# Kernel tuning notes

Measured on AMD Instinct MI355X. Metric: run time of the kernel, lower is better.

## Reference

```python
import jax, jax.numpy as jnp
import numpy as np

N = 40000      # nodes (adj.size(0))
ISIZE = 64     # feature dim
K = 24         # kept kNN neighbors per node after d_cut mask
E = N * K      # learner candidate edges
E_ADJ = N * K  # GCN adjacency edges
OMEGA = 0.9
GAMMA = 2.0
D_CUT = 1.5


def setup_inputs() -> dict:
    key = jax.random.key(0)
    k = jax.random.split(key, 8)
    features = jax.random.normal(k[0], (N, ISIZE), jnp.float32)
    sc = 1.0 / np.sqrt(ISIZE)
    W1 = jax.random.normal(k[1], (ISIZE, ISIZE), jnp.float32) * sc
    b1 = jnp.zeros((ISIZE,), jnp.float32)
    W2 = jax.random.normal(k[2], (ISIZE, ISIZE), jnp.float32) * sc
    b2 = jnp.zeros((ISIZE,), jnp.float32)
    adj_row = jax.random.randint(k[3], (E_ADJ,), 0, N, dtype=jnp.int32)
    adj_col = jax.random.randint(k[4], (E_ADJ,), 0, N, dtype=jnp.int32)
    # kNN-style candidate edges: K neighbors per node, no self loops
    i_idx = jnp.repeat(jnp.arange(N, dtype=jnp.int32), K)
    j_idx = (i_idx + jax.random.randint(k[5], (E,), 1, N, dtype=jnp.int32)) % N
    # precomputed distance prior: s_d = 1/exp(gamma*(d/d_cut)^2)
    dist = jax.random.uniform(k[6], (E,), jnp.float32, 0.1, 2.0)
    s_d = jnp.exp(-GAMMA * (dist / D_CUT) ** 2)
    return {"features": features, "W1": W1, "b1": b1, "W2": W2, "b2": b2,
            "s_d": s_d, "adj_row": adj_row, "adj_col": adj_col,
            "i_idx": i_idx, "j_idx": j_idx}


def _gcn(x, W, b, row, col):
    """PyG GCNConv: symmetric norm with self loops, aggregate src=row into dst=col."""
    xw = x @ W
    deg = 1.0 + jax.ops.segment_sum(jnp.ones((row.shape[0],), jnp.float32), col,
                                    num_segments=N)
    dinv = jax.lax.rsqrt(deg)
    msg = (dinv[row] * dinv[col])[:, None] * xw[row]            # [E_ADJ, ISIZE]
    out = jax.ops.segment_sum(msg, col, num_segments=N)
    return out + (dinv * dinv)[:, None] * xw + b                # self-loop + bias


def reference(features, W1, b1, W2, b2, s_d, adj_row, adj_col, i_idx, j_idx):
    # GCN stack (nlayers=2), ReLU between layers
    h = jax.nn.relu(_gcn(features, W1, b1, adj_row, adj_col))
    h = _gcn(h, W2, b2, adj_row, adj_col)
    # F.normalize(h, p=2, dim=-1)
    h = h / jnp.maximum(jnp.linalg.norm(h, axis=-1, keepdims=True), 1e-12)
    # per-edge cosine scores, clamped at 0, blended with distance prior
    s_val = jnp.sum(h[i_idx] * h[j_idx], axis=-1)               # [E]
    s_val = jax.nn.relu(s_val)
    s_val = OMEGA * s_val + (1.0 - OMEGA) * s_d
    # SparseTensor.to_symmetric(reduce='mean'): average with reverse edge if present
    keys = i_idx * N + j_idx                                    # fits int32 (N=4e4)
    rkeys = j_idx * N + i_idx
    order = jnp.argsort(keys)
    sk = keys[order]
    pos = jnp.clip(jnp.searchsorted(sk, rkeys), 0, E - 1)
    found = sk[pos] == rkeys
    rev = order[pos]
    v_sym = jnp.where(found, 0.5 * (s_val + s_val[rev]), s_val)
    # symmetric COO: original edges + reverse copies (zeroed where reverse existed)
    rows_s = jnp.concatenate([i_idx, j_idx])                    # [2E]
    cols_s = jnp.concatenate([j_idx, i_idx])
    vals_s = jnp.concatenate([v_sym, jnp.where(found, 0.0, v_sym)])
    # normalize_adj_symm: D^{-1/2} S D^{-1/2}
    deg = jax.ops.segment_sum(vals_s, rows_s, num_segments=N)
    dinv = jnp.where(deg > 0, jax.lax.rsqrt(jnp.maximum(deg, 1e-12)), 0.0)
    vals_norm = dinv[rows_s] * vals_s * dinv[cols_s]
    return vals_norm, vals_s
```

## Files before the change

kernel.cpp:

```cpp
#include <hip/hip_runtime.h>

#define N_NODES 40000
#define ISIZE   64
#define KNN     24
#define NE      (N_NODES * KNN)
#define OMEGA   0.9f
#define CAP     64
#define NBUCK   80
#define BCAP    16384
#define JBCAP   16384
#define EPT     8

__device__ __forceinline__ float bf2f(unsigned short s) {
    return __uint_as_float(((unsigned)s) << 16);
}
__device__ __forceinline__ unsigned short f2bf(float f) {
    unsigned u = __float_as_uint(f);
    u += 0x7fffu + ((u >> 16) & 1u);
    return (unsigned short)(u >> 16);
}
__device__ __forceinline__ float bflo(unsigned u) { return __uint_as_float(u << 16); }
__device__ __forceinline__ float bfhi(unsigned u) { return __uint_as_float(u & 0xffff0000u); }
__device__ __forceinline__ unsigned pack2(float lo, float hi) {
    return (unsigned)f2bf(lo) | ((unsigned)f2bf(hi) << 16);
}

__global__ void k_mega1(const float* __restrict__ X, const float* __restrict__ W,
                        unsigned short* __restrict__ Y0, unsigned short* __restrict__ Y1,
                        const int* __restrict__ row, const int* __restrict__ col,
                        const int* __restrict__ j_idx,
                        int* __restrict__ bcnt, unsigned* __restrict__ bbuf,
                        unsigned* __restrict__ ovf2, int* __restrict__ ovf2_cnt,
                        int* __restrict__ jbcnt, unsigned* __restrict__ jbbuf,
                        unsigned* __restrict__ jovf, int* __restrict__ jovf_cnt,
                        unsigned char* __restrict__ revb) {
    __shared__ float sW[64 * 64];
    __shared__ float sX[32 * 64];
    const int GB  = N_NODES / 32;
    const int NBA = (NE + 256 * EPT - 1) / (256 * EPT);
    int bx = blockIdx.x;
    int tid = threadIdx.x;
    if (bx < GB) {
        int row0 = bx * 32;
        for (int t = tid; t < 1024; t += 256)
            ((float4*)sW)[t] = ((const float4*)W)[t];
        for (int t = tid; t < 512; t += 256)
            ((float4*)sX)[t] = ((const float4*)(X + row0 * 64))[t];
        __syncthreads();
        int cc = tid & 63;
        int rl = tid >> 6;
        for (int r = rl; r < 32; r += 4) {
            float acc = 0.0f;
#pragma unroll
            for (int kk = 0; kk < 64; kk++) acc += sX[r * 64 + kk] * sW[kk * 64 + cc];
            if (cc < 32) Y0[(row0 + r) * 32 + cc]      = f2bf(acc);
            else         Y1[(row0 + r) * 32 + cc - 32] = f2bf(acc);
        }
    } else if (bx < GB + 2 * NBA) {
        int* lcnt  = (int*)sW;
        int* lbase = lcnt + NBUCK;
        int blk = bx - GB;
        bool adj = blk < NBA;
        if (!adj) blk -= NBA;
        for (int b = tid; b < NBUCK; b += 256) lcnt[b] = 0;
        __syncthreads();
        int e0 = blk * (256 * EPT);
        int myslot[EPT]; int myb[EPT]; unsigned myp[EPT];
        for (int k = 0; k < EPT; k++) {
            int e = e0 + k * 256 + tid;
            if (e < NE) {
                int b; unsigned p;
                if (adj) { int r = row[e], c = col[e]; b = c >> 9; p = ((unsigned)r << 16) | (unsigned)c; }
                else     { int j = j_idx[e];           b = j >> 9; p = ((unsigned)(j & 511) << 20) | (unsigned)e; }
                myb[k] = b; myp[k] = p;
                myslot[k] = atomicAdd(&lcnt[b], 1);
            } else myb[k] = -1;
        }
        __syncthreads();
        int* gcnt = adj ? bcnt : jbcnt;
        for (int b = tid; b < NBUCK; b += 256)
            lbase[b] = (lcnt[b] > 0) ? atomicAdd(&gcnt[b], lcnt[b]) : 0;
        __syncthreads();
        unsigned* gbuf = adj ? bbuf : jbbuf;
        unsigned* govf = adj ? ovf2 : jovf;
        int* gocnt = adj ? ovf2_cnt : jovf_cnt;
        for (int k = 0; k < EPT; k++) {
            if (myb[k] < 0) continue;
            int pos = lbase[myb[k]] + myslot[k];
            if (pos < BCAP) gbuf[myb[k] * BCAP + pos] = myp[k];
            else { int p = atomicAdd(gocnt, 1); govf[p] = myp[k]; }
        }
    } else {
        int e = (bx - GB - 2 * NBA) * 256 + tid;
        int i = e / KNN;
        int j = j_idx[e];
        const uint4* jj4 = (const uint4*)(j_idx + j * KNN);
        int rt = 255;
#pragma unroll
        for (int k = 5; k >= 0; k--) {
            uint4 u = jj4[k];
            if ((int)u.w == i) rt = 4 * k + 3;
            if ((int)u.z == i) rt = 4 * k + 2;
            if ((int)u.y == i) rt = 4 * k + 1;
            if ((int)u.x == i) rt = 4 * k + 0;
        }
        revb[e] = (unsigned char)rt;
    }
}

__global__ void k_scatter3(const unsigned* __restrict__ bbuf, const int* __restrict__ bcnt,
                           int* __restrict__ cnt, unsigned short* __restrict__ ebuf,
                           unsigned* __restrict__ ovf, int* __restrict__ ovf_cnt,
                           const unsigned* __restrict__ ovf2, const int* __restrict__ ovf2_cnt) {
    __shared__ int lcnt2[512];
    int b = blockIdx.x;
    int tid = threadIdx.x;
    if (tid < 512) lcnt2[tid] = 0;
    __syncthreads();
    int n = min(bcnt[b], BCAP);
    for (int idx = tid; idx < n; idx += 1024) {
        unsigned p = bbuf[b * BCAP + idx];
        int c = (int)(p & 0xffffu), r = (int)(p >> 16);
        int slot = atomicAdd(&lcnt2[c & 511], 1);
        if (slot < CAP) ebuf[c * CAP + slot] = (unsigned short)r;
        else { int q = atomicAdd(ovf_cnt, 1); ovf[q] = p; }
    }
    int m = ovf2_cnt[0];
    for (int idx = tid; idx < m; idx += 1024) {
        unsigned p = ovf2[idx];
        int c = (int)(p & 0xffffu), r = (int)(p >> 16);
        if ((c >> 9) != b) continue;
        int slot = atomicAdd(&lcnt2[c & 511], 1);
        if (slot < CAP) ebuf[c * CAP + slot] = (unsigned short)r;
        else { int q = atomicAdd(ovf_cnt, 1); ovf[q] = p; }
    }
    __syncthreads();
    if (tid < 512) {
        int node = b * 512 + tid;
        if (node < N_NODES) cnt[node] = lcnt2[tid];
    }
}

__global__ void __launch_bounds__(1024, 1)
k_aggemm1(const uint4* __restrict__ X0q, const uint4* __restrict__ X1q,
          const float* __restrict__ W2,
          unsigned short* __restrict__ C0, unsigned short* __restrict__ C1,
          const int* __restrict__ cnt,
          const unsigned short* __restrict__ ebuf, const float* __restrict__ bias,
          const unsigned* __restrict__ ovf, const int* __restrict__ ovf_cnt) {
    __shared__ float sW[64 * 64];
    __shared__ float sB[32 * 64];
    int tid  = threadIdx.x;
    int lane = tid & 63;
    int half = lane >> 5, sl = lane & 31;
    int nl = (tid >> 6) * 2 + half;
    int n  = blockIdx.x * 32 + nl;

    ((float4*)sW)[tid] = ((const float4*)W2)[tid];

    int deg = cnt[n];
    int bucketed = min(deg, CAP);
    int nb0 = min(bucketed, 32);
    int nb1 = bucketed - nb0;

    int   r0v = 0, r1v = 0;
    float d0v = 0.0f, d1v = 0.0f;
    if (sl < nb0) { r0v = (int)ebuf[n * CAP + sl];      d0v = rsqrtf(1.0f + (float)cnt[r0v]); }
    if (sl < nb1) { r1v = (int)ebuf[n * CAP + 32 + sl]; d1v = rsqrtf(1.0f + (float)cnt[r1v]); }

    int g = sl >> 2;
    int f = sl & 3;

    float a[16];
#pragma unroll
    for (int k = 0; k < 16; k++) a[k] = 0.f;
    int np0 = (nb0 + 7) >> 3;
    int np1 = (nb1 + 7) >> 3;

#pragma unroll 4
    for (int d = 0; d < np0; d++) {
        int   q = 8 * d + g;
        int   r = __shfl(r0v, q, 32);
        float c = __shfl(d0v, q, 32);
        uint4 u0 = X0q[r * 4 + f];
        uint4 u1 = X1q[r * 4 + f];
        a[0]  += c * bflo(u0.x); a[1]  += c * bfhi(u0.x);
        a[2]  += c * bflo(u0.y); a[3]  += c * bfhi(u0.y);
        a[4]  += c * bflo(u0.z); a[5]  += c * bfhi(u0.z);
        a[6]  += c * bflo(u0.w); a[7]  += c * bfhi(u0.w);
        a[8]  += c * bflo(u1.x); a[9]  += c * bfhi(u1.x);
        a[10] += c * bflo(u1.y); a[11] += c * bfhi(u1.y);
        a[12] += c * bflo(u1.z); a[13] += c * bfhi(u1.z);
        a[14] += c * bflo(u1.w); a[15] += c * bfhi(u1.w);
    }
#pragma unroll 4
    for (int d = 0; d < np1; d++) {
        int   q = 8 * d + g;
        int   r = __shfl(r1v, q, 32);
        float c = __shfl(d1v, q, 32);
        uint4 u0 = X0q[r * 4 + f];
        uint4 u1 = X1q[r * 4 + f];
        a[0]  += c * bflo(u0.x); a[1]  += c * bfhi(u0.x);
        a[2]  += c * bflo(u0.y); a[3]  += c * bfhi(u0.y);
        a[4]  += c * bflo(u0.z); a[5]  += c * bfhi(u0.z);
        a[6]  += c * bflo(u0.w); a[7]  += c * bfhi(u0.w);
        a[8]  += c * bflo(u1.x); a[9]  += c * bfhi(u1.x);
        a[10] += c * bflo(u1.y); a[11] += c * bfhi(u1.y);
        a[12] += c * bflo(u1.z); a[13] += c * bfhi(u1.z);
        a[14] += c * bflo(u1.w); a[15] += c * bfhi(u1.w);
    }
    if (deg > CAP) {
        int m = ovf_cnt[0];
        for (int k2 = 0; k2 < m; k2++) {
            unsigned p = ovf[k2];
            if ((int)(p & 0xffffu) == n && g == 0) {
                int r = (int)(p >> 16);
                float c = rsqrtf(1.0f + (float)cnt[r]);
                uint4 u0 = X0q[r * 4 + f], u1 = X1q[r * 4 + f];
                a[0]  += c * bflo(u0.x); a[1]  += c * bfhi(u0.x);
                a[2]  += c * bflo(u0.y); a[3]  += c * bfhi(u0.y);
                a[4]  += c * bflo(u0.z); a[5]  += c * bfhi(u0.z);
                a[6]  += c * bflo(u0.w); a[7]  += c * bfhi(u0.w);
                a[8]  += c * bflo(u1.x); a[9]  += c * bfhi(u1.x);
                a[10] += c * bflo(u1.y); a[11] += c * bfhi(u1.y);
                a[12] += c * bflo(u1.z); a[13] += c * bfhi(u1.z);
                a[14] += c * bflo(u1.w); a[15] += c * bfhi(u1.w);
            }
        }
    }
#pragma unroll
    for (int k = 0; k < 16; k++) {
        a[k] += __shfl_xor(a[k], 4, 32);
        a[k] += __shfl_xor(a[k], 8, 32);
        a[k] += __shfl_xor(a[k], 16, 32);
    }

    float di = rsqrtf(1.0f + (float)deg);
    float dd = di * di;
    uint4 s0 = X0q[n * 4 + f], s1 = X1q[n * 4 + f];
    float4 bA0 = ((const float4*)bias)[2 * f];
    float4 bA1 = ((const float4*)bias)[2 * f + 1];
    float4 bB0 = ((const float4*)(bias + 32))[2 * f];
    float4 bB1 = ((const float4*)(bias + 32))[2 * f + 1];
    if (g == 0) {
        float* dst = sB + nl * 64 + 8 * f;
        dst[0] = fmaxf(di * a[0]  + dd * bflo(s0.x) + bA0.x, 0.f);
        dst[1] = fmaxf(di * a[1]  + dd * bfhi(s0.x) + bA0.y, 0.f);
        dst[2] = fmaxf(di * a[2]  + dd * bflo(s0.y) + bA0.z, 0.f);
        dst[3] = fmaxf(di * a[3]  + dd * bfhi(s0.y) + bA0.w, 0.f);
        dst[4] = fmaxf(di * a[4]  + dd * bflo(s0.z) + bA1.x, 0.f);
        dst[5] = fmaxf(di * a[5]  + dd * bfhi(s0.z) + bA1.y, 0.f);
        dst[6] = fmaxf(di * a[6]  + dd * bflo(s0.w) + bA1.z, 0.f);
        dst[7] = fmaxf(di * a[7]  + dd * bfhi(s0.w) + bA1.w, 0.f);
        float* dst2 = dst + 32;
        dst2[0] = fmaxf(di * a[8]  + dd * bflo(s1.x) + bB0.x, 0.f);
        dst2[1] = fmaxf(di * a[9]  + dd * bfhi(s1.x) + bB0.y, 0.f);
        dst2[2] = fmaxf(di * a[10] + dd * bflo(s1.y) + bB0.z, 0.f);
        dst2[3] = fmaxf(di * a[11] + dd * bfhi(s1.y) + bB0.w, 0.f);
        dst2[4] = fmaxf(di * a[12] + dd * bflo(s1.z) + bB1.x, 0.f);
        dst2[5] = fmaxf(di * a[13] + dd * bfhi(s1.z) + bB1.y, 0.f);
        dst2[6] = fmaxf(di * a[14] + dd * bflo(s1.w) + bB1.z, 0.f);
        dst2[7] = fmaxf(di * a[15] + dd * bfhi(s1.w) + bB1.w, 0.f);
    }
    __syncthreads();

    int col = tid & 63;
    int r0  = tid >> 6;
    float acc0 = 0.f, acc1 = 0.f;
#pragma unroll
    for (int kk = 0; kk < 64; kk++) {
        float wv = sW[kk * 64 + col];
        acc0 += sB[r0 * 64 + kk] * wv;
        acc1 += sB[(r0 + 16) * 64 + kk] * wv;
    }
    int na = blockIdx.x * 32 + r0;
    int nb = na + 16;
    if (col < 32) {
        C0[na * 32 + col] = f2bf(acc0);
        C0[nb * 32 + col] = f2bf(acc1);
    } else {
        C1[na * 32 + col - 32] = f2bf(acc0);
        C1[nb * 32 + col - 32] = f2bf(acc1);
    }
}

__global__ void k_aggf4(const uint4* __restrict__ X0q, const uint4* __restrict__ X1q,
                        uint4* __restrict__ O0q, uint4* __restrict__ O1q,
                        const int* __restrict__ cnt,
                        const unsigned short* __restrict__ ebuf, const float* __restrict__ bias,
                        const unsigned* __restrict__ ovf, const int* __restrict__ ovf_cnt) {
    int w = (blockIdx.x * 256 + threadIdx.x) >> 6;
    int lane = threadIdx.x & 63;
    int half = lane >> 5, sl = lane & 31;
    int n = w * 2 + half;
    if (n >= N_NODES) return;
    int deg = cnt[n];
    int bucketed = min(deg, CAP);
    int nb0 = min(bucketed, 32);
    int nb1 = bucketed - nb0;

    int   r0v = 0, r1v = 0;
    float d0v = 0.0f, d1v = 0.0f;
    if (sl < nb0) { r0v = (int)ebuf[n * CAP + sl];      d0v = rsqrtf(1.0f + (float)cnt[r0v]); }
    if (sl < nb1) { r1v = (int)ebuf[n * CAP + 32 + sl]; d1v = rsqrtf(1.0f + (float)cnt[r1v]); }

    int g = sl >> 2;
    int f = sl & 3;

    float a[16];
#pragma unroll
    for (int k = 0; k < 16; k++) a[k] = 0.f;
    int np0 = (nb0 + 7) >> 3;
    int np1 = (nb1 + 7) >> 3;

#pragma unroll 4
    for (int d = 0; d < np0; d++) {
        int   q = 8 * d + g;
        int   r = __shfl(r0v, q, 32);
        float c = __shfl(d0v, q, 32);
        uint4 u0 = X0q[r * 4 + f];
        uint4 u1 = X1q[r * 4 + f];
        a[0]  += c * bflo(u0.x); a[1]  += c * bfhi(u0.x);
        a[2]  += c * bflo(u0.y); a[3]  += c * bfhi(u0.y);
        a[4]  += c * bflo(u0.z); a[5]  += c * bfhi(u0.z);
        a[6]  += c * bflo(u0.w); a[7]  += c * bfhi(u0.w);
        a[8]  += c * bflo(u1.x); a[9]  += c * bfhi(u1.x);
        a[10] += c * bflo(u1.y); a[11] += c * bfhi(u1.y);
        a[12] += c * bflo(u1.z); a[13] += c * bfhi(u1.z);
        a[14] += c * bflo(u1.w); a[15] += c * bfhi(u1.w);
    }
#pragma unroll 4
    for (int d = 0; d < np1; d++) {
        int   q = 8 * d + g;
        int   r = __shfl(r1v, q, 32);
        float c = __shfl(d1v, q, 32);
        uint4 u0 = X0q[r * 4 + f];
        uint4 u1 = X1q[r * 4 + f];
        a[0]  += c * bflo(u0.x); a[1]  += c * bfhi(u0.x);
        a[2]  += c * bflo(u0.y); a[3]  += c * bfhi(u0.y);
        a[4]  += c * bflo(u0.z); a[5]  += c * bfhi(u0.z);
        a[6]  += c * bflo(u0.w); a[7]  += c * bfhi(u0.w);
        a[8]  += c * bflo(u1.x); a[9]  += c * bfhi(u1.x);
        a[10] += c * bflo(u1.y); a[11] += c * bfhi(u1.y);
        a[12] += c * bflo(u1.z); a[13] += c * bfhi(u1.z);
        a[14] += c * bflo(u1.w); a[15] += c * bfhi(u1.w);
    }
    if (deg > CAP) {
        int m = ovf_cnt[0];
        for (int k2 = 0; k2 < m; k2++) {
            unsigned p = ovf[k2];
            if ((int)(p & 0xffffu) == n && g == 0) {
                int r = (int)(p >> 16);
                float c = rsqrtf(1.0f + (float)cnt[r]);
                uint4 u0 = X0q[r * 4 + f], u1 = X1q[r * 4 + f];
                a[0]  += c * bflo(u0.x); a[1]  += c * bfhi(u0.x);
                a[2]  += c * bflo(u0.y); a[3]  += c * bfhi(u0.y);
                a[4]  += c * bflo(u0.z); a[5]  += c * bfhi(u0.z);
                a[6]  += c * bflo(u0.w); a[7]  += c * bfhi(u0.w);
                a[8]  += c * bflo(u1.x); a[9]  += c * bfhi(u1.x);
                a[10] += c * bflo(u1.y); a[11] += c * bfhi(u1.y);
                a[12] += c * bflo(u1.z); a[13] += c * bfhi(u1.z);
                a[14] += c * bflo(u1.w); a[15] += c * bfhi(u1.w);
            }
        }
    }
#pragma unroll
    for (int k = 0; k < 16; k++) {
        a[k] += __shfl_xor(a[k], 4, 32);
        a[k] += __shfl_xor(a[k], 8, 32);
        a[k] += __shfl_xor(a[k], 16, 32);
    }

    float di = rsqrtf(1.0f + (float)deg);
    float dd = di * di;
    uint4 s0 = X0q[n * 4 + f], s1 = X1q[n * 4 + f];
    float4 bA0 = ((const float4*)bias)[2 * f];
    float4 bA1 = ((const float4*)bias)[2 * f + 1];
    float4 bB0 = ((const float4*)(bias + 32))[2 * f];
    float4 bB1 = ((const float4*)(bias + 32))[2 * f + 1];
    float v[16];
    v[0]  = di * a[0]  + dd * bflo(s0.x) + bA0.x;
    v[1]  = di * a[1]  + dd * bfhi(s0.x) + bA0.y;
    v[2]  = di * a[2]  + dd * bflo(s0.y) + bA0.z;
    v[3]  = di * a[3]  + dd * bfhi(s0.y) + bA0.w;
    v[4]  = di * a[4]  + dd * bflo(s0.z) + bA1.x;
    v[5]  = di * a[5]  + dd * bfhi(s0.z) + bA1.y;
    v[6]  = di * a[6]  + dd * bflo(s0.w) + bA1.z;
    v[7]  = di * a[7]  + dd * bfhi(s0.w) + bA1.w;
    v[8]  = di * a[8]  + dd * bflo(s1.x) + bB0.x;
    v[9]  = di * a[9]  + dd * bfhi(s1.x) + bB0.y;
    v[10] = di * a[10] + dd * bflo(s1.y) + bB0.z;
    v[11] = di * a[11] + dd * bfhi(s1.y) + bB0.w;
    v[12] = di * a[12] + dd * bflo(s1.z) + bB1.x;
    v[13] = di * a[13] + dd * bfhi(s1.z) + bB1.y;
    v[14] = di * a[14] + dd * bflo(s1.w) + bB1.z;
    v[15] = di * a[15] + dd * bfhi(s1.w) + bB1.w;

    float s = 0.f;
#pragma unroll
    for (int k = 0; k < 16; k++) s += v[k] * v[k];
    s += __shfl_xor(s, 1, 32);
    s += __shfl_xor(s, 2, 32);
    float inv = 1.0f / fmaxf(sqrtf(s), 1e-12f);
#pragma unroll
    for (int k = 0; k < 16; k++) v[k] *= inv;
    if (g == 0) {
        O0q[n * 4 + f] = make_uint4(pack2(v[0], v[1]),  pack2(v[2], v[3]),
                                    pack2(v[4], v[5]),  pack2(v[6], v[7]));
        O1q[n * 4 + f] = make_uint4(pack2(v[8], v[9]),  pack2(v[10], v[11]),
                                    pack2(v[12], v[13]), pack2(v[14], v[15]));
    }
}

__global__ void k_dotsym(const uint4* __restrict__ H0q, const uint4* __restrict__ H1q,
                         const float* __restrict__ s_d, const int* __restrict__ j_idx,
                         const unsigned char* __restrict__ revb,
                         float* __restrict__ outS) {
    int t = blockIdx.x * 256 + threadIdx.x;
    int e = t >> 2;
    int f = t & 3;
    int i = e / KNN;
    int j = j_idx[e];
    uint4 a0 = H0q[i * 4 + f];
    uint4 b0 = H0q[j * 4 + f];
    uint4 a1 = H1q[i * 4 + f];
    uint4 b1 = H1q[j * 4 + f];
    float s = bflo(a0.x) * bflo(b0.x) + bfhi(a0.x) * bfhi(b0.x)
            + bflo(a0.y) * bflo(b0.y) + bfhi(a0.y) * bfhi(b0.y)
            + bflo(a0.z) * bflo(b0.z) + bfhi(a0.z) * bfhi(b0.z)
            + bflo(a0.w) * bflo(b0.w) + bfhi(a0.w) * bfhi(b0.w)
            + bflo(a1.x) * bflo(b1.x) + bfhi(a1.x) * bfhi(b1.x)
            + bflo(a1.y) * bflo(b1.y) + bfhi(a1.y) * bfhi(b1.y)
            + bflo(a1.z) * bflo(b1.z) + bfhi(a1.z) * bfhi(b1.z)
            + bflo(a1.w) * bflo(b1.w) + bfhi(a1.w) * bfhi(b1.w);
    s += __shfl_xor(s, 1);
    s += __shfl_xor(s, 2);
    if (f == 0) {
        float base = OMEGA * fmaxf(s, 0.0f);
        int rt = revb[e];
        float vv, v2;
        if (rt != 255) {
            int rev = j * KNN + rt;
            vv = base + 0.5f * (1.0f - OMEGA) * (s_d[e] + s_d[rev]);
            v2 = 0.0f;
        } else {
            vv = base + (1.0f - OMEGA) * s_d[e];
            v2 = vv;
        }
        outS[e] = vv;
        outS[NE + e] = v2;
    }
}

__global__ void k_jagg(const unsigned* __restrict__ jbbuf, const int* __restrict__ jbcnt,
                       const float* __restrict__ outS, float* __restrict__ dinv2,
                       const unsigned* __restrict__ jovf, const int* __restrict__ jovf_cnt,
                       const int* __restrict__ j_idx) {
    __shared__ float ld[512];
    int b = blockIdx.x;
    int tid = threadIdx.x;
    if (tid < 512) ld[tid] = 0.0f;
    __syncthreads();
    const float* outSv2 = outS + NE;
    int n = min(jbcnt[b], JBCAP);
    for (int idx = tid; idx < n; idx += 1024) {
        unsigned p = jbbuf[b * JBCAP + idx];
        atomicAdd(&ld[p >> 20], outSv2[p & 0xFFFFFu]);
    }
    int m = jovf_cnt[0];
    for (int t2 = tid; t2 < m; t2 += 1024) {
        int e = (int)(jovf[t2] & 0xFFFFFu);
        int j = j_idx[e];
        if ((j >> 9) == b) atomicAdd(&ld[j & 511], outSv2[e]);
    }
    __syncthreads();
    if (tid < 512) {
        int node = b * 512 + tid;
        if (node < N_NODES) {
            float d = ld[tid];
            const float* pp = outS + node * KNN;
#pragma unroll
            for (int qq = 0; qq < KNN; qq++) d += pp[qq];
            dinv2[node] = (d > 0.0f) ? rsqrtf(fmaxf(d, 1e-12f)) : 0.0f;
        }
    }
}

__global__ void k_norm(const float* __restrict__ outS, const float* __restrict__ dinv2,
                       const int* __restrict__ j_idx, float* __restrict__ out) {
    int t = blockIdx.x * 256 + threadIdx.x;
    int r, c;
    if (t < NE) { r = t / KNN; c = j_idx[t]; }
    else        { int e = t - NE; r = j_idx[e]; c = e / KNN; }
    out[t] = dinv2[r] * outS[t] * dinv2[c];
}

extern "C" void kernel_launch(void* const* d_in, const int* in_sizes, int n_in,
                              void* d_out, int out_size, void* d_ws, size_t ws_size,
                              hipStream_t stream) {
    const float* features = (const float*)d_in[0];
    const float* W1       = (const float*)d_in[1];
    const float* b1       = (const float*)d_in[2];
    const float* W2       = (const float*)d_in[3];
    const float* b2       = (const float*)d_in[4];
    const float* s_d      = (const float*)d_in[5];
    const int*   adj_row  = (const int*)d_in[6];
    const int*   adj_col  = (const int*)d_in[7];
    const int*   j_idx    = (const int*)d_in[9];
    float* out = (float*)d_out;

    const int N32 = N_NODES * 32;
    int*   cnt     = (int*)d_ws;
    int*   ovfcnts = cnt + N_NODES;
    int*   bcnt    = ovfcnts + 16;
    int*   jbcnt   = bcnt + NBUCK;
    float* dinv2   = (float*)(jbcnt + NBUCK);
    unsigned short* A0  = (unsigned short*)(dinv2 + N_NODES);
    unsigned short* A1  = A0 + N32;
    unsigned short* C0  = A1 + N32;
    unsigned short* C1  = C0 + N32;
    unsigned short* H0  = C1 + N32;
    unsigned short* H1  = H0 + N32;
    unsigned short* ebuf = H1 + N32;
    unsigned* ovf    = (unsigned*)(ebuf + N_NODES * CAP);
    unsigned char* revb = (unsigned char*)(ovf + NE);
    unsigned* bbuf   = (unsigned*)(revb + NE);
    unsigned* jbbuf  = bbuf + NBUCK * BCAP;
    unsigned* ovf2   = jbbuf + NBUCK * JBCAP;
    unsigned* jovf   = ovf2 + NE;

    size_t zero_bytes = (size_t)(N_NODES + 16 + 2 * NBUCK) * 4;
    hipMemsetAsync(cnt, 0, zero_bytes, stream);

    const int GB = N_NODES / 32;
    const int NBA = (NE + 256 * EPT - 1) / (256 * EPT);
    const int RB = NE / 256;
    k_mega1<<<GB + 2 * NBA + RB, 256, 0, stream>>>(
        features, W1, A0, A1, adj_row, adj_col, j_idx,
        bcnt, bbuf, ovf2, ovfcnts + 4, jbcnt, jbbuf, jovf, ovfcnts + 8, revb);

    k_scatter3<<<NBUCK, 1024, 0, stream>>>(bbuf, bcnt, cnt, ebuf,
                                           ovf, ovfcnts, ovf2, ovfcnts + 4);

    k_aggemm1<<<N_NODES / 32, 1024, 0, stream>>>(
        (const uint4*)A0, (const uint4*)A1, W2, C0, C1,
        cnt, ebuf, b1, ovf, ovfcnts);

    k_aggf4<<<(N_NODES / 2 * 64 + 255) / 256, 256, 0, stream>>>(
        (const uint4*)C0, (const uint4*)C1, (uint4*)H0, (uint4*)H1,
        cnt, ebuf, b2, ovf, ovfcnts);

    float* outS = out + 2 * NE;
    k_dotsym<<<NE * 4 / 256, 256, 0, stream>>>(
        (const uint4*)H0, (const uint4*)H1, s_d, j_idx, revb, outS);

    k_jagg<<<NBUCK, 1024, 0, stream>>>(jbbuf, jbcnt, outS, dinv2, jovf, ovfcnts + 8, j_idx);
    k_norm<<<2 * NE / 256, 256, 0, stream>>>(outS, dinv2, j_idx, out);
}
```

Baseline: 236.4 us.

## Interleave split bf16 feature halves into one 64-wide row layout

Replaces the two separate 32-column bf16 arrays (A0/A1, C0/C1, H0/H1) with single 64-column row-major arrays, so each node's features occupy one contiguous 128-byte row. Gathers in the aggregation kernels then touch one cache-line region per neighbor instead of two separate arrays. The edge dot-product kernel also changes from 4 to 2 threads per edge, with each thread loading four uint4 values, which halves the thread count and removes one shuffle step. This trades some parallelism in k_dotsym for fewer threads and better gather locality.

New measurement: 235.4 us (median of 2 runs). No clear change (-0.4%).

```diff
diff --git a/kernel.cpp b/kernel.cpp
--- a/kernel.cpp
+++ b/kernel.cpp
@@ -24,9 +24,15 @@
 __device__ __forceinline__ unsigned pack2(float lo, float hi) {
     return (unsigned)f2bf(lo) | ((unsigned)f2bf(hi) << 16);
 }
+__device__ __forceinline__ float dot8(uint4 a, uint4 b) {
+    return bflo(a.x) * bflo(b.x) + bfhi(a.x) * bfhi(b.x)
+         + bflo(a.y) * bflo(b.y) + bfhi(a.y) * bfhi(b.y)
+         + bflo(a.z) * bflo(b.z) + bfhi(a.z) * bfhi(b.z)
+         + bflo(a.w) * bflo(b.w) + bfhi(a.w) * bfhi(b.w);
+}
 
 __global__ void k_mega1(const float* __restrict__ X, const float* __restrict__ W,
-                        unsigned short* __restrict__ Y0, unsigned short* __restrict__ Y1,
+                        unsigned short* __restrict__ Y,
                         const int* __restrict__ row, const int* __restrict__ col,
                         const int* __restrict__ j_idx,
                         int* __restrict__ bcnt, unsigned* __restrict__ bbuf,
@@ -53,8 +59,7 @@
             float acc = 0.0f;
 #pragma unroll
             for (int kk = 0; kk < 64; kk++) acc += sX[r * 64 + kk] * sW[kk * 64 + cc];
-            if (cc < 32) Y0[(row0 + r) * 32 + cc]      = f2bf(acc);
-            else         Y1[(row0 + r) * 32 + cc - 32] = f2bf(acc);
+            Y[(row0 + r) * 64 + cc] = f2bf(acc);
         }
     } else if (bx < GB + 2 * NBA) {
         int* lcnt  = (int*)sW;
@@ -142,9 +147,8 @@
 }
 
 __global__ void __launch_bounds__(1024, 1)
-k_aggemm1(const uint4* __restrict__ X0q, const uint4* __restrict__ X1q,
-          const float* __restrict__ W2,
-          unsigned short* __restrict__ C0, unsigned short* __restrict__ C1,
+k_aggemm1(const uint4* __restrict__ Aq, const float* __restrict__ W2,
+          unsigned short* __restrict__ C,
           const int* __restrict__ cnt,
           const unsigned short* __restrict__ ebuf, const float* __restrict__ bias,
           const unsigned* __restrict__ ovf, const int* __restrict__ ovf_cnt) {
@@ -182,8 +186,8 @@
         int   q = 8 * d + g;
         int   r = __shfl(r0v, q, 32);
         float c = __shfl(d0v, q, 32);
-        uint4 u0 = X0q[r * 4 + f];
-        uint4 u1 = X1q[r * 4 + f];
+        uint4 u0 = Aq[r * 8 + f];
+        uint4 u1 = Aq[r * 8 + 4 + f];
         a[0]  += c * bflo(u0.x); a[1]  += c * bfhi(u0.x);
         a[2]  += c * bflo(u0.y); a[3]  += c * bfhi(u0.y);
         a[4]  += c * bflo(u0.z); a[5]  += c * bfhi(u0.z);
@@ -198,8 +202,8 @@
         int   q = 8 * d + g;
         int   r = __shfl(r1v, q, 32);
         float c = __shfl(d1v, q, 32);
-        uint4 u0 = X0q[r * 4 + f];
-        uint4 u1 = X1q[r * 4 + f];
+        uint4 u0 = Aq[r * 8 + f];
+        uint4 u1 = Aq[r * 8 + 4 + f];
         a[0]  += c * bflo(u0.x); a[1]  += c * bfhi(u0.x);
         a[2]  += c * bflo(u0.y); a[3]  += c * bfhi(u0.y);
         a[4]  += c * bflo(u0.z); a[5]  += c * bfhi(u0.z);
@@ -216,7 +220,7 @@
             if ((int)(p & 0xffffu) == n && g == 0) {
                 int r = (int)(p >> 16);
                 float c = rsqrtf(1.0f + (float)cnt[r]);
-                uint4 u0 = X0q[r * 4 + f], u1 = X1q[r * 4 + f];
+                uint4 u0 = Aq[r * 8 + f], u1 = Aq[r * 8 + 4 + f];
                 a[0]  += c * bflo(u0.x); a[1]  += c * bfhi(u0.x);
                 a[2]  += c * bflo(u0.y); a[3]  += c * bfhi(u0.y);
                 a[4]  += c * bflo(u0.z); a[5]  += c * bfhi(u0.z);
@@ -237,7 +241,7 @@
 
     float di = rsqrtf(1.0f + (float)deg);
     float dd = di * di;
-    uint4 s0 = X0q[n * 4 + f], s1 = X1q[n * 4 + f];
+    uint4 s0 = Aq[n * 8 + f], s1 = Aq[n * 8 + 4 + f];
     float4 bA0 = ((const float4*)bias)[2 * f];
     float4 bA1 = ((const float4*)bias)[2 * f + 1];
     float4 bB0 = ((const float4*)(bias + 32))[2 * f];
@@ -274,18 +278,11 @@
         acc1 += sB[(r0 + 16) * 64 + kk] * wv;
     }
     int na = blockIdx.x * 32 + r0;
-    int nb = na + 16;
-    if (col < 32) {
-        C0[na * 32 + col] = f2bf(acc0);
-        C0[nb * 32 + col] = f2bf(acc1);
-    } else {
-        C1[na * 32 + col - 32] = f2bf(acc0);
-        C1[nb * 32 + col - 32] = f2bf(acc1);
-    }
-}
-
-__global__ void k_aggf4(const uint4* __restrict__ X0q, const uint4* __restrict__ X1q,
-                        uint4* __restrict__ O0q, uint4* __restrict__ O1q,
+    C[na * 64 + col]        = f2bf(acc0);
+    C[(na + 16) * 64 + col] = f2bf(acc1);
+}
+
+__global__ void k_aggf4(const uint4* __restrict__ Cq, uint4* __restrict__ Hq,
                         const int* __restrict__ cnt,
                         const unsigned short* __restrict__ ebuf, const float* __restrict__ bias,
                         const unsigned* __restrict__ ovf, const int* __restrict__ ovf_cnt) {
@@ -318,8 +315,8 @@
         int   q = 8 * d + g;
         int   r = __shfl(r0v, q, 32);
         float c = __shfl(d0v, q, 32);
-        uint4 u0 = X0q[r * 4 + f];
-        uint4 u1 = X1q[r * 4 + f];
+        uint4 u0 = Cq[r * 8 + f];
+        uint4 u1 = Cq[r * 8 + 4 + f];
         a[0]  += c * bflo(u0.x); a[1]  += c * bfhi(u0.x);
         a[2]  += c * bflo(u0.y); a[3]  += c * bfhi(u0.y);
         a[4]  += c * bflo(u0.z); a[5]  += c * bfhi(u0.z);
@@ -334,8 +331,8 @@
         int   q = 8 * d + g;
         int   r = __shfl(r1v, q, 32);
         float c = __shfl(d1v, q, 32);
-        uint4 u0 = X0q[r * 4 + f];
-        uint4 u1 = X1q[r * 4 + f];
+        uint4 u0 = Cq[r * 8 + f];
+        uint4 u1 = Cq[r * 8 + 4 + f];
         a[0]  += c * bflo(u0.x); a[1]  += c * bfhi(u0.x);
         a[2]  += c * bflo(u0.y); a[3]  += c * bfhi(u0.y);
         a[4]  += c * bflo(u0.z); a[5]  += c * bfhi(u0.z);
@@ -352,7 +349,7 @@
             if ((int)(p & 0xffffu) == n && g == 0) {
                 int r = (int)(p >> 16);
                 float c = rsqrtf(1.0f + (float)cnt[r]);
-                uint4 u0 = X0q[r * 4 + f], u1 = X1q[r * 4 + f];
+                uint4 u0 = Cq[r * 8 + f], u1 = Cq[r * 8 + 4 + f];
                 a[0]  += c * bflo(u0.x); a[1]  += c * bfhi(u0.x);
                 a[2]  += c * bflo(u0.y); a[3]  += c * bfhi(u0.y);
                 a[4]  += c * bflo(u0.z); a[5]  += c * bfhi(u0.z);
@@ -373,7 +370,7 @@
 
     float di = rsqrtf(1.0f + (float)deg);
     float dd = di * di;
-    uint4 s0 = X0q[n * 4 + f], s1 = X1q[n * 4 + f];
+    uint4 s0 = Cq[n * 8 + f], s1 = Cq[n * 8 + 4 + f];
     float4 bA0 = ((const float4*)bias)[2 * f];
     float4 bA1 = ((const float4*)bias)[2 * f + 1];
     float4 bB0 = ((const float4*)(bias + 32))[2 * f];
@@ -405,36 +402,28 @@
 #pragma unroll
     for (int k = 0; k < 16; k++) v[k] *= inv;
     if (g == 0) {
-        O0q[n * 4 + f] = make_uint4(pack2(v[0], v[1]),  pack2(v[2], v[3]),
-                                    pack2(v[4], v[5]),  pack2(v[6], v[7]));
-        O1q[n * 4 + f] = make_uint4(pack2(v[8], v[9]),  pack2(v[10], v[11]),
-                                    pack2(v[12], v[13]), pack2(v[14], v[15]));
-    }
-}
-
-__global__ void k_dotsym(const uint4* __restrict__ H0q, const uint4* __restrict__ H1q,
+        Hq[n * 8 + f]     = make_uint4(pack2(v[0], v[1]),  pack2(v[2], v[3]),
+                                       pack2(v[4], v[5]),  pack2(v[6], v[7]));
+        Hq[n * 8 + 4 + f] = make_uint4(pack2(v[8], v[9]),  pack2(v[10], v[11]),
+                                       pack2(v[12], v[13]), pack2(v[14], v[15]));
+    }
+}
+
+__global__ void k_dotsym(const uint4* __restrict__ Hq,
                          const float* __restrict__ s_d, const int* __restrict__ j_idx,
                          const unsigned char* __restrict__ revb,
                          float* __restrict__ outS) {
     int t = blockIdx.x * 256 + threadIdx.x;
-    int e = t >> 2;
-    int f = t & 3;
+    int e = t >> 1;
+    int f = t & 1;
     int i = e / KNN;
     int j = j_idx[e];
-    uint4 a0 = H0q[i * 4 + f];
-    uint4 b0 = H0q[j * 4 + f];
-    uint4 a1 = H1q[i * 4 + f];
-    uint4 b1 = H1q[j * 4 + f];
-    float s = bflo(a0.x) * bflo(b0.x) + bfhi(a0.x) * bfhi(b0.x)
-            + bflo(a0.y) * bflo(b0.y) + bfhi(a0.y) * bfhi(b0.y)
-            + bflo(a0.z) * bflo(b0.z) + bfhi(a0.z) * bfhi(b0.z)
-            + bflo(a0.w) * bflo(b0.w) + bfhi(a0.w) * bfhi(b0.w)
-            + bflo(a1.x) * bflo(b1.x) + bfhi(a1.x) * bfhi(b1.x)
-            + bflo(a1.y) * bflo(b1.y) + bfhi(a1.y) * bfhi(b1.y)
-            + bflo(a1.z) * bflo(b1.z) + bfhi(a1.z) * bfhi(b1.z)
-            + bflo(a1.w) * bflo(b1.w) + bfhi(a1.w) * bfhi(b1.w);
+    const uint4* Hi = Hq + i * 8 + 4 * f;
+    const uint4* Hj = Hq + j * 8 + 4 * f;
+    uint4 a0 = Hi[0], a1 = Hi[1], a2 = Hi[2], a3 = Hi[3];
+    uint4 b0 = Hj[0], b1 = Hj[1], b2 = Hj[2], b3 = Hj[3];
+    float s = dot8(a0, b0) + dot8(a1, b1) + dot8(a2, b2) + dot8(a3, b3);
     s += __shfl_xor(s, 1);
-    s += __shfl_xor(s, 2);
     if (f == 0) {
         float base = OMEGA * fmaxf(s, 0.0f);
         int rt = revb[e];
@@ -509,19 +498,16 @@
     const int*   j_idx    = (const int*)d_in[9];
     float* out = (float*)d_out;
 
-    const int N32 = N_NODES * 32;
+    const int N64 = N_NODES * 64;
     int*   cnt     = (int*)d_ws;
     int*   ovfcnts = cnt + N_NODES;
     int*   bcnt    = ovfcnts + 16;
     int*   jbcnt   = bcnt + NBUCK;
     float* dinv2   = (float*)(jbcnt + NBUCK);
-    unsigned short* A0  = (unsigned short*)(dinv2 + N_NODES);
-    unsigned short* A1  = A0 + N32;
-    unsigned short* C0  = A1 + N32;
-    unsigned short* C1  = C0 + N32;
-    unsigned short* H0  = C1 + N32;
-    unsigned short* H1  = H0 + N32;
-    unsigned short* ebuf = H1 + N32;
+    unsigned short* A   = (unsigned short*)(dinv2 + N_NODES);
+    unsigned short* C   = A + N64;
+    unsigned short* H   = C + N64;
+    unsigned short* ebuf = H + N64;
     unsigned* ovf    = (unsigned*)(ebuf + N_NODES * CAP);
     unsigned char* revb = (unsigned char*)(ovf + NE);
     unsigned* bbuf   = (unsigned*)(revb + NE);
@@ -536,23 +522,21 @@
     const int NBA = (NE + 256 * EPT - 1) / (256 * EPT);
     const int RB = NE / 256;
     k_mega1<<<GB + 2 * NBA + RB, 256, 0, stream>>>(
-        features, W1, A0, A1, adj_row, adj_col, j_idx,
+        features, W1, A, adj_row, adj_col, j_idx,
         bcnt, bbuf, ovf2, ovfcnts + 4, jbcnt, jbbuf, jovf, ovfcnts + 8, revb);
 
     k_scatter3<<<NBUCK, 1024, 0, stream>>>(bbuf, bcnt, cnt, ebuf,
                                            ovf, ovfcnts, ovf2, ovfcnts + 4);
 
     k_aggemm1<<<N_NODES / 32, 1024, 0, stream>>>(
-        (const uint4*)A0, (const uint4*)A1, W2, C0, C1,
-        cnt, ebuf, b1, ovf, ovfcnts);
+        (const uint4*)A, W2, C, cnt, ebuf, b1, ovf, ovfcnts);
 
     k_aggf4<<<(N_NODES / 2 * 64 + 255) / 256, 256, 0, stream>>>(
-        (const uint4*)C0, (const uint4*)C1, (uint4*)H0, (uint4*)H1,
-        cnt, ebuf, b2, ovf, ovfcnts);
+        (const uint4*)C, (uint4*)H, cnt, ebuf, b2, ovf, ovfcnts);
 
     float* outS = out + 2 * NE;
-    k_dotsym<<<NE * 4 / 256, 256, 0, stream>>>(
-        (const uint4*)H0, (const uint4*)H1, s_d, j_idx, revb, outS);
+    k_dotsym<<<NE * 2 / 256, 256, 0, stream>>>(
+        (const uint4*)H, s_d, j_idx, revb, outS);
 
     k_jagg<<<NBUCK, 1024, 0, stream>>>(jbbuf, jbcnt, outS, dinv2, jovf, ovfcnts + 8, j_idx);
     k_norm<<<2 * NE / 256, 256, 0, stream>>>(outS, dinv2, j_idx, out);
```
